# Performance work log

Measured on AMD Instinct MI355X. Metric: run time of the kernel, lower is better.

The kernel has to match this reference:

```python
import jax, jax.numpy as jnp
import numpy as np

HID, NH, QLR, KVLR, QK, VH, RH = 7168, 128, 1536, 512, 128, 128, 64
EPS = 1.1920929e-07  # torch.finfo(float32).eps, RMSNorm eps=None default
ROPE_BASE = 10000.0


def _rmsnorm(x, w):
    return x * jax.lax.rsqrt(jnp.mean(x * x, axis=-1, keepdims=True) + EPS) * w


def _rope_tables(seq_len, dim):
    inv_freq = 1.0 / (ROPE_BASE ** (np.arange(0, dim, 2, dtype=np.float32) / dim))
    t = np.arange(seq_len, dtype=np.float32)
    freqs = np.outer(t, inv_freq)          # [S, dim/2]
    emb = np.concatenate([freqs, freqs], -1)  # [S, dim]
    return jnp.asarray(np.cos(emb)), jnp.asarray(np.sin(emb))


def _apply_rope(x, cos, sin):
    # x: [B, H, S, D]; rotate-half convention matching the torch module
    d = x.shape[-1]
    x1, x2 = x[..., : d // 2], x[..., d // 2 :]
    rotated = jnp.concatenate([-x2, x1], axis=-1)
    return x * cos + rotated * sin


def setup_inputs() -> dict:
    key = jax.random.key(0)
    ks = jax.random.split(key, 9)
    def w(k, out_dim, in_dim):
        return jax.random.normal(k, (out_dim, in_dim), jnp.float32) / np.sqrt(in_dim)
    return {
        "hidden_states": jax.random.normal(ks[0], (1, 1024, HID), jnp.float32),
        "w_q_down": w(ks[1], QLR, HID),
        "q_norm_w": jnp.ones((QLR,), jnp.float32),
        "w_q_up": w(ks[2], NH * (QK + RH), QLR),
        "w_kv_down": w(ks[3], KVLR + RH, HID),
        "kv_norm_w": jnp.ones((KVLR,), jnp.float32),
        "w_kv_up": w(ks[4], NH * (QK + VH), KVLR),
        "w_out": w(ks[5], HID, NH * VH),
    }


def reference(hidden_states, w_q_down, q_norm_w, w_q_up, w_kv_down, kv_norm_w, w_kv_up, w_out):
    B, S, _ = hidden_states.shape
    cos, sin = _rope_tables(S, RH)

    # Q path: down -> RMSNorm -> up, split into non-rope / rope parts
    c_q = jnp.einsum("bsh,qh->bsq", hidden_states, w_q_down)            # [B,S,QLR]
    q_cr = jnp.einsum("bsq,oq->bso", _rmsnorm(c_q, q_norm_w), w_q_up)   # [B,S,NH*(QK+RH)]
    q_cr = q_cr.reshape(B, S, NH, QK + RH).transpose(0, 2, 1, 3)        # [B,NH,S,QK+RH]
    q_c, q_r = q_cr[..., :QK], q_cr[..., QK:]

    # KV path: shared latent + MQA rope key
    ckv_kr = jnp.einsum("bsh,oh->bso", hidden_states, w_kv_down)        # [B,S,KVLR+RH]
    c_kv, k_r = ckv_kr[..., :KVLR], ckv_kr[..., KVLR:]
    k_r = k_r[:, None, :, :]                                            # [B,1,S,RH]
    kv = jnp.einsum("bsq,oq->bso", _rmsnorm(c_kv, kv_norm_w), w_kv_up)  # [B,S,NH*(QK+VH)]
    kv = kv.reshape(B, S, NH, QK + VH).transpose(0, 2, 1, 3)            # [B,NH,S,QK+VH]
    k_c, v = kv[..., :QK], kv[..., QK:]

    q_r = _apply_rope(q_r, cos, sin)
    k_r = _apply_rope(k_r, cos, sin)

    q = jnp.concatenate([q_c, q_r], axis=-1)                            # [B,NH,S,QK+RH]
    k = jnp.concatenate([k_c, jnp.broadcast_to(k_r, (B, NH, S, RH))], axis=-1)

    scale = 1.0 / np.sqrt(QK + RH)
    scores = jnp.einsum("bhqd,bhkd->bhqk", q, k) * scale
    attn = jax.nn.softmax(scores, axis=-1)
    o = jnp.einsum("bhqk,bhkd->bhqd", attn, v)                          # [B,NH,S,VH]
    o = o.transpose(0, 2, 1, 3).reshape(B, S, NH * VH)
    return jnp.einsum("bso,ho->bsh", o, w_out)
```

## Files before the change

kernel.cpp:

```cpp
#include <hip/hip_runtime.h>
#include <hip/hip_bf16.h>
#include <math.h>

#define HIDN 7168
#define NHEAD 128
#define QLRANK 1536
#define KVLRANK 512
#define QKD 128
#define VHD 128
#define RHD 64
#define SEQ 1024
#define RMS_EPS 1.1920929e-07f

typedef unsigned short u16;
typedef __attribute__((ext_vector_type(8))) short bf16x8;
typedef __attribute__((ext_vector_type(4))) float f32x4;
typedef __attribute__((ext_vector_type(8))) unsigned short u16x8;

__device__ __forceinline__ u16 f2bf(float f) {
    unsigned int u = __float_as_uint(f);
    unsigned int r = (u + 0x7FFFu + ((u >> 16) & 1u)) >> 16;
    return (u16)r;
}
__device__ __forceinline__ float bf2f(u16 v) {
    return __uint_as_float(((unsigned int)v) << 16);
}

__device__ __forceinline__ void gld_lds16(const u16* g, u16* l) {
    __builtin_amdgcn_global_load_lds(
        (const __attribute__((address_space(1))) unsigned int*)g,
        (__attribute__((address_space(3))) unsigned int*)l,
        16, 0, 0);
}

__global__ __launch_bounds__(256) void f32_to_bf16(const float* __restrict__ in,
                                                   u16* __restrict__ out, long n) {
    long i = ((long)blockIdx.x * blockDim.x + threadIdx.x) * 8;
    long stride = (long)gridDim.x * blockDim.x * 8;
    for (; i < n; i += stride) {
        float4 a = *(const float4*)(in + i);
        float4 b = *(const float4*)(in + i + 4);
        u16x8 o;
        o[0] = f2bf(a.x); o[1] = f2bf(a.y); o[2] = f2bf(a.z); o[3] = f2bf(a.w);
        o[4] = f2bf(b.x); o[5] = f2bf(b.y); o[6] = f2bf(b.z); o[7] = f2bf(b.w);
        *(u16x8*)(out + i) = o;
    }
}

template <int OUT_BF16>
__global__ __launch_bounds__(256) void gemm_bt(const u16* __restrict__ A,
                                               const u16* __restrict__ B,
                                               void* __restrict__ Cv,
                                               int M, int N, int Kslice, long ldk) {
    __shared__ u16 As[2 * 128 * 64];
    __shared__ u16 Bs[2 * 128 * 64];
    const int tid = threadIdx.x;
    const int lane = tid & 63;
    const int w = tid >> 6;
    const int wr = w >> 1, wc = w & 1;
    const int l15 = lane & 15, lg = lane >> 4;
    const int n0 = blockIdx.x * 128;
    const int m0 = blockIdx.y * 128;
    const long kbase = (long)blockIdx.z * Kslice;

    const u16* asrc[4];
    const u16* bsrc[4];
    int aoff[4];
#pragma unroll
    for (int i = 0; i < 4; ++i) {
        int r = (w * 4 + i) * 8 + (lane >> 3);
        int gc = (lane & 7) ^ (r & 7);
        asrc[i] = A + (long)(m0 + r) * ldk + kbase + gc * 8;
        int br = n0 + r; if (br >= N) br = N - 1;
        bsrc[i] = B + (long)br * ldk + kbase + gc * 8;
        aoff[i] = (w * 4 + i) * 512;
    }

    f32x4 acc[4][4];
    const f32x4 z = {0.f, 0.f, 0.f, 0.f};
#pragma unroll
    for (int i = 0; i < 4; ++i)
#pragma unroll
        for (int j = 0; j < 4; ++j) acc[i][j] = z;

    auto stage = [&](int bufi, int kofs) {
#pragma unroll
        for (int i = 0; i < 4; ++i) {
            gld_lds16(asrc[i] + kofs, As + bufi * 8192 + aoff[i]);
            gld_lds16(bsrc[i] + kofs, Bs + bufi * 8192 + aoff[i]);
        }
    };

    const int nsteps = Kslice >> 6;
    stage(0, 0);
    asm volatile("s_waitcnt vmcnt(0)" ::: "memory");
    __builtin_amdgcn_s_barrier();

    int cur = 0;
    for (int t = 0; t < nsteps; ++t) {
        if (t + 1 < nsteps) stage(cur ^ 1, (t + 1) * 64);
        const u16* Ab = As + cur * 8192;
        const u16* Bb = Bs + cur * 8192;
#pragma unroll
        for (int kk = 0; kk < 2; ++kk) {
            bf16x8 a[4], b[4];
#pragma unroll
            for (int i = 0; i < 4; ++i) {
                int row = wr * 64 + i * 16 + l15;
                a[i] = *(const bf16x8*)&Ab[row * 64 + ((kk * 4 + lg) ^ (row & 7)) * 8];
            }
#pragma unroll
            for (int j = 0; j < 4; ++j) {
                int row = wc * 64 + j * 16 + l15;
                b[j] = *(const bf16x8*)&Bb[row * 64 + ((kk * 4 + lg) ^ (row & 7)) * 8];
            }
#pragma unroll
            for (int i = 0; i < 4; ++i)
#pragma unroll
                for (int j = 0; j < 4; ++j)
                    acc[i][j] = __builtin_amdgcn_mfma_f32_16x16x32_bf16(a[i], b[j], acc[i][j], 0, 0, 0);
        }
        asm volatile("s_waitcnt vmcnt(0)" ::: "memory");
        __builtin_amdgcn_s_barrier();
        cur ^= 1;
    }

#pragma unroll
    for (int i = 0; i < 4; ++i)
#pragma unroll
        for (int j = 0; j < 4; ++j)
#pragma unroll
            for (int r = 0; r < 4; ++r) {
                int m = m0 + wr * 64 + i * 16 + lg * 4 + r;
                int n = n0 + wc * 64 + j * 16 + l15;
                if (n < N) {
                    if (OUT_BF16)
                        ((u16*)Cv)[(long)m * N + n] = f2bf(acc[i][j][r]);
                    else
                        ((float*)Cv)[(long)blockIdx.z * M * N + (long)m * N + n] = acc[i][j][r];
                }
            }
}

__global__ __launch_bounds__(256) void reduce_parts(const float* __restrict__ parts,
                                                    float* __restrict__ out,
                                                    int nparts, long mn) {
    long i = ((long)blockIdx.x * 256 + threadIdx.x) * 4;
    long stride = (long)gridDim.x * 256 * 4;
    for (; i < mn; i += stride) {
        float4 s = *(const float4*)(parts + i);
        for (int p = 1; p < nparts; ++p) {
            float4 v = *(const float4*)(parts + (long)p * mn + i);
            s.x += v.x; s.y += v.y; s.z += v.z; s.w += v.w;
        }
        *(float4*)(out + i) = s;
    }
}

__global__ __launch_bounds__(256) void rmsnorm_kernel(const float* __restrict__ x,
                                                      const float* __restrict__ w,
                                                      u16* __restrict__ y,
                                                      int stride, int norm_len) {
    const int row = blockIdx.x;
    const float* xr = x + (long)row * stride;
    float ss = 0.f;
    for (int i = threadIdx.x; i < norm_len; i += 256) {
        float v = xr[i];
        ss += v * v;
    }
#pragma unroll
    for (int off = 32; off > 0; off >>= 1) ss += __shfl_down(ss, off);
    __shared__ float partial[4];
    if ((threadIdx.x & 63) == 0) partial[threadIdx.x >> 6] = ss;
    __syncthreads();
    float tot = partial[0] + partial[1] + partial[2] + partial[3];
    float rs = 1.0f / sqrtf(tot / (float)norm_len + RMS_EPS);
    u16* yr = y + (long)row * norm_len;
    for (int i = threadIdx.x; i < norm_len; i += 256) yr[i] = f2bf(xr[i] * rs * w[i]);
}

__global__ void rope_tables(float* __restrict__ cos_t, float* __restrict__ sin_t) {
    int s = blockIdx.x;
    int i = threadIdx.x;
    float invf = powf(10000.0f, -((float)(2 * i) / 64.0f));
    float ang = (float)s * invf;
    cos_t[s * 32 + i] = cosf(ang);
    sin_t[s * 32 + i] = sinf(ang);
}

__global__ void rope_q(u16* __restrict__ q_cr, const float* __restrict__ cos_t,
                       const float* __restrict__ sin_t) {
    int s = blockIdx.x;
    int h = blockIdx.y * 2 + (threadIdx.x >> 5);
    int i = threadIdx.x & 31;
    u16* base = q_cr + (s * (NHEAD * 192) + h * 192 + QKD);
    float x1 = bf2f(base[i]);
    float x2 = bf2f(base[i + 32]);
    float c = cos_t[s * 32 + i], sn = sin_t[s * 32 + i];
    base[i]      = f2bf(x1 * c - x2 * sn);
    base[i + 32] = f2bf(x2 * c + x1 * sn);
}

__global__ void rope_k(const float* __restrict__ ckv_kr, const float* __restrict__ cos_t,
                       const float* __restrict__ sin_t, u16* __restrict__ kr) {
    int s = blockIdx.x;
    int i = threadIdx.x;
    if (i < 32) {
        const float* base = ckv_kr + (s * 576 + 512);
        float x1 = base[i], x2 = base[i + 32];
        float c = cos_t[s * 32 + i], sn = sin_t[s * 32 + i];
        kr[s * 64 + i]      = f2bf(x1 * c - x2 * sn);
        kr[s * 64 + i + 32] = f2bf(x2 * c + x1 * sn);
    }
}

__global__ __launch_bounds__(256) void build_vt(const u16* __restrict__ kv,
                                                u16* __restrict__ vT) {
    __shared__ u16 vtile[64][136];
    const int h = blockIdx.x, sb = blockIdx.y, s0 = sb * 64;
    const int tid = threadIdx.x;
#pragma unroll
    for (int it = 0; it < 4; ++it) {
        int c = it * 256 + tid;
        int row = c >> 4;
        int off8 = (c & 15) * 8;
        *(u16x8*)&vtile[row][off8] =
            *(const u16x8*)&kv[(s0 + row) * 32768 + h * 256 + 128 + off8];
    }
    __syncthreads();
    const int sl = tid & 63;
    const int dvb = tid >> 6;
#pragma unroll
    for (int it = 0; it < 32; ++it) {
        int dv = dvb + it * 4;
        vT[(h * 128 + dv) * 1024 + s0 + sl] = vtile[sl][dv];
    }
}

__global__ __launch_bounds__(512) void mla_attn(const u16* __restrict__ q_cr,
                                                const u16* __restrict__ kv,
                                                const u16* __restrict__ kr,
                                                const u16* __restrict__ vT,
                                                u16* __restrict__ o_g) {
    __shared__ u16 ks[64][200];
    __shared__ u16 vts[128][72];
    __shared__ u16 p_lds[8][16][72];
    const int qb = blockIdx.x, h = blockIdx.y;
    const int s0q = qb * 128;
    const int tid = threadIdx.x, lane = tid & 63, w = tid >> 6;
    const int l15 = lane & 15, lg = lane >> 4;
    const float scale = 0.07216878364870323f;

    bf16x8 qreg[6];
    {
        const int qrow = s0q + w * 16 + l15;
#pragma unroll
        for (int kk = 0; kk < 6; ++kk)
            qreg[kk] = *(const bf16x8*)&q_cr[qrow * (NHEAD * 192) + h * 192 + kk * 32 + lg * 8];
    }

    const int krow0 = tid >> 4,           koff0 = (tid & 15) * 8;
    const int krow1 = (512 + tid) >> 4,   koff1 = ((512 + tid) & 15) * 8;
    const int rrow  = tid >> 3,           roff  = (tid & 7) * 8;
    const int vdv0  = tid >> 3,           voff0 = (tid & 7) * 8;
    const int vdv1  = (512 + tid) >> 3,   voff1 = ((512 + tid) & 7) * 8;
    const u16* kvp = kv + h * 256;
    const u16* vtp = vT + (long)(h * 128) * 1024;

    u16x8 kreg0, kreg1, krreg, vreg0, vreg1;
    auto load_tile = [&](int s0k) {
        kreg0 = *(const u16x8*)&kvp[(long)(s0k + krow0) * 32768 + koff0];
        kreg1 = *(const u16x8*)&kvp[(long)(s0k + krow1) * 32768 + koff1];
        krreg = *(const u16x8*)&kr[(s0k + rrow) * 64 + roff];
        vreg0 = *(const u16x8*)&vtp[(long)vdv0 * 1024 + s0k + voff0];
        vreg1 = *(const u16x8*)&vtp[(long)vdv1 * 1024 + s0k + voff1];
    };

    f32x4 o_acc[8];
    const f32x4 z = {0.f, 0.f, 0.f, 0.f};
#pragma unroll
    for (int d = 0; d < 8; ++d) o_acc[d] = z;
    float m_r[4], l_r[4];
#pragma unroll
    for (int r = 0; r < 4; ++r) { m_r[r] = -1e30f; l_r[r] = 0.f; }

    load_tile(0);

    for (int kt = 0; kt < 16; ++kt) {
        __syncthreads();
        *(u16x8*)&ks[krow0][koff0]      = kreg0;
        *(u16x8*)&ks[krow1][koff1]      = kreg1;
        *(u16x8*)&ks[rrow][128 + roff]  = krreg;
        *(u16x8*)&vts[vdv0][voff0]      = vreg0;
        *(u16x8*)&vts[vdv1][voff1]      = vreg1;
        __syncthreads();
        if (kt + 1 < 16) load_tile((kt + 1) * 64);

        f32x4 sf[4];
#pragma unroll
        for (int j = 0; j < 4; ++j) sf[j] = z;
#pragma unroll
        for (int kk = 0; kk < 6; ++kk) {
            bf16x8 a = qreg[kk];
#pragma unroll
            for (int j = 0; j < 4; ++j) {
                bf16x8 b = *(const bf16x8*)&ks[j * 16 + l15][kk * 32 + lg * 8];
                sf[j] = __builtin_amdgcn_mfma_f32_16x16x32_bf16(a, b, sf[j], 0, 0, 0);
            }
        }

        float p[4][4];
        float alpha[4];
#pragma unroll
        for (int r = 0; r < 4; ++r) {
            float mx = fmaxf(fmaxf(sf[0][r], sf[1][r]), fmaxf(sf[2][r], sf[3][r]));
#pragma unroll
            for (int off = 1; off < 16; off <<= 1) mx = fmaxf(mx, __shfl_xor(mx, off));
            mx *= scale;
            float mnew = fmaxf(m_r[r], mx);
            alpha[r] = __expf(m_r[r] - mnew);
            float rs = 0.f;
#pragma unroll
            for (int j = 0; j < 4; ++j) {
                float pv = __expf(sf[j][r] * scale - mnew);
                p[j][r] = pv;
                rs += pv;
            }
#pragma unroll
            for (int off = 1; off < 16; off <<= 1) rs += __shfl_xor(rs, off);
            l_r[r] = l_r[r] * alpha[r] + rs;
            m_r[r] = mnew;
        }
#pragma unroll
        for (int d = 0; d < 8; ++d)
#pragma unroll
            for (int r = 0; r < 4; ++r) o_acc[d][r] *= alpha[r];

#pragma unroll
        for (int j = 0; j < 4; ++j)
#pragma unroll
            for (int r = 0; r < 4; ++r)
                p_lds[w][lg * 4 + r][j * 16 + l15] = f2bf(p[j][r]);

#pragma unroll
        for (int kk2 = 0; kk2 < 2; ++kk2) {
            bf16x8 a = *(const bf16x8*)&p_lds[w][l15][kk2 * 32 + lg * 8];
#pragma unroll
            for (int d = 0; d < 8; ++d) {
                bf16x8 b = *(const bf16x8*)&vts[d * 16 + l15][kk2 * 32 + lg * 8];
                o_acc[d] = __builtin_amdgcn_mfma_f32_16x16x32_bf16(a, b, o_acc[d], 0, 0, 0);
            }
        }
    }

#pragma unroll
    for (int d = 0; d < 8; ++d)
#pragma unroll
        for (int r = 0; r < 4; ++r) {
            int srow = s0q + w * 16 + lg * 4 + r;
            float v = o_acc[d][r] / l_r[r];
            o_g[srow * 16384 + h * 128 + d * 16 + l15] = f2bf(v);
        }
}

extern "C" void kernel_launch(void* const* d_in, const int* in_sizes, int n_in,
                              void* d_out, int out_size, void* d_ws, size_t ws_size,
                              hipStream_t stream) {
    const float* hs        = (const float*)d_in[0];
    const float* w_q_down  = (const float*)d_in[1];
    const float* q_norm_w  = (const float*)d_in[2];
    const float* w_q_up    = (const float*)d_in[3];
    const float* w_kv_down = (const float*)d_in[4];
    const float* kv_norm_w = (const float*)d_in[5];
    const float* w_kv_up   = (const float*)d_in[6];
    const float* w_out     = (const float*)d_in[7];
    float* out = (float*)d_out;
    char* ws = (char*)d_ws;

    const size_t SZ_HS   = (size_t)SEQ * HIDN * 2;
    const size_t SZ_KV   = (size_t)SEQ * 32768 * 2;
    const size_t SZ_QCR  = (size_t)SEQ * (NHEAD * 192) * 2;
    const size_t SZ_VT   = (size_t)NHEAD * 128 * 1024 * 2;
    const size_t SZ_WB   = (size_t)24576 * 1536 * 2;
    const size_t SZ_CQ   = (size_t)SEQ * QLRANK * 4;
    const size_t SZ_CQN  = (size_t)SEQ * QLRANK * 2;
    const size_t SZ_CKV  = (size_t)SEQ * 576 * 4;
    const size_t SZ_CKVN = (size_t)SEQ * KVLRANK * 2;
    const size_t SZ_KR   = (size_t)SEQ * 64 * 2;
    const size_t SZ_OG   = (size_t)SEQ * 16384 * 2;
    const size_t SZ_TAB  = (size_t)SEQ * 32 * 4;

    size_t off = 0;
    u16* hs_bf  = (u16*)(ws + off); off += SZ_HS;
    u16* kvb    = (u16*)(ws + off); off += SZ_KV;
    u16* q_cr   = (u16*)(ws + off); off += SZ_QCR;
    u16* vT     = (u16*)(ws + off); off += SZ_VT;
    u16* W_BUF  = (u16*)(ws + off); off += SZ_WB;
    float* parts = (float*)((char*)W_BUF + 33554432);
    u16* wout_bf = (u16*)ws;
    float* c_q    = (float*)(ws + off); off += SZ_CQ;
    u16* cq_n     = (u16*)(ws + off); off += SZ_CQN;
    float* ckv_kr = (float*)(ws + off); off += SZ_CKV;
    u16* ckv_n    = (u16*)(ws + off); off += SZ_CKVN;
    u16* kr       = (u16*)(ws + off); off += SZ_KR;
    u16* o_g      = (u16*)(ws + off); off += SZ_OG;
    float* cos_t  = (float*)(ws + off); off += SZ_TAB;
    float* sin_t  = (float*)(ws + off); off += SZ_TAB;
    const size_t SZ_POP = (size_t)2 * SEQ * HIDN * 4;
    float* parts_op = (float*)(ws + off);
    const bool splitOP = (off + SZ_POP) <= ws_size;
    (void)in_sizes; (void)n_in; (void)out_size;

    rope_tables<<<dim3(SEQ), dim3(32), 0, stream>>>(cos_t, sin_t);
    f32_to_bf16<<<2048, 256, 0, stream>>>(hs, hs_bf, (long)SEQ * HIDN);

    f32_to_bf16<<<2048, 256, 0, stream>>>(w_q_down, W_BUF, (long)QLRANK * HIDN);
    gemm_bt<0><<<dim3(QLRANK / 128, SEQ / 128, 4), 256, 0, stream>>>(hs_bf, W_BUF, parts, SEQ, QLRANK, HIDN / 4, HIDN);
    reduce_parts<<<1024, 256, 0, stream>>>(parts, c_q, 4, (long)SEQ * QLRANK);
    rmsnorm_kernel<<<SEQ, 256, 0, stream>>>(c_q, q_norm_w, cq_n, QLRANK, QLRANK);

    f32_to_bf16<<<2048, 256, 0, stream>>>(w_q_up, W_BUF, (long)24576 * QLRANK);
    gemm_bt<1><<<dim3(24576 / 128, SEQ / 128), 256, 0, stream>>>(cq_n, W_BUF, q_cr, SEQ, 24576, QLRANK, QLRANK);

    f32_to_bf16<<<2048, 256, 0, stream>>>(w_kv_down, W_BUF, (long)576 * HIDN);
    gemm_bt<0><<<dim3(5, SEQ / 128, 8), 256, 0, stream>>>(hs_bf, W_BUF, parts, SEQ, 576, HIDN / 8, HIDN);
    reduce_parts<<<1024, 256, 0, stream>>>(parts, ckv_kr, 8, (long)SEQ * 576);
    rmsnorm_kernel<<<SEQ, 256, 0, stream>>>(ckv_kr, kv_norm_w, ckv_n, 576, KVLRANK);
    rope_k<<<SEQ, 64, 0, stream>>>(ckv_kr, cos_t, sin_t, kr);

    f32_to_bf16<<<2048, 256, 0, stream>>>(w_kv_up, W_BUF, (long)32768 * KVLRANK);
    gemm_bt<1><<<dim3(32768 / 128, SEQ / 128), 256, 0, stream>>>(ckv_n, W_BUF, kvb, SEQ, 32768, KVLRANK, KVLRANK);

    rope_q<<<dim3(SEQ, NHEAD / 2), 64, 0, stream>>>(q_cr, cos_t, sin_t);
    build_vt<<<dim3(NHEAD, SEQ / 64), 256, 0, stream>>>(kvb, vT);

    mla_attn<<<dim3(SEQ / 128, NHEAD), 512, 0, stream>>>(q_cr, kvb, kr, vT, o_g);

    f32_to_bf16<<<2048, 256, 0, stream>>>(w_out, wout_bf, (long)HIDN * 16384);
    if (splitOP) {
        gemm_bt<0><<<dim3(HIDN / 128, SEQ / 128, 2), 256, 0, stream>>>(o_g, wout_bf, parts_op, SEQ, HIDN, 16384 / 2, 16384);
        reduce_parts<<<1024, 256, 0, stream>>>(parts_op, out, 2, (long)SEQ * HIDN);
    } else {
        gemm_bt<0><<<dim3(HIDN / 128, SEQ / 128), 256, 0, stream>>>(o_g, wout_bf, out, SEQ, HIDN, 16384, 16384);
    }
}
```

Baseline: 1.022 ms.

## Deepen GEMM LDS pipeline to four stages and drop split-K for out-proj

The shared GEMM kernel moves from a double-buffered LDS pipeline to a four-buffer ring. Three k-tiles stay in flight, and partial vmcnt waits replace the full drain on every iteration, so more global-load latency is hidden. The output projection no longer uses the 2-way split-K with a separate reduction pass and writes straight to the output. The weight conversion grid for that projection is also enlarged. LDS use per block grows to 128KB, which may limit occupancy to one block per CU.

```diff
diff --git a/kernel.cpp b/kernel.cpp
--- a/kernel.cpp
+++ b/kernel.cpp
@@ -52,8 +52,8 @@
                                                const u16* __restrict__ B,
                                                void* __restrict__ Cv,
                                                int M, int N, int Kslice, long ldk) {
-    __shared__ u16 As[2 * 128 * 64];
-    __shared__ u16 Bs[2 * 128 * 64];
+    __shared__ u16 As[4 * 128 * 64];
+    __shared__ u16 Bs[4 * 128 * 64];
     const int tid = threadIdx.x;
     const int lane = tid & 63;
     const int w = tid >> 6;
@@ -83,24 +83,30 @@
 #pragma unroll
         for (int j = 0; j < 4; ++j) acc[i][j] = z;
 
-    auto stage = [&](int bufi, int kofs) {
+    auto stage = [&](int t) {
+        const int bb = (t & 3) * 8192;
+        const long ko = (long)t * 64;
 #pragma unroll
         for (int i = 0; i < 4; ++i) {
-            gld_lds16(asrc[i] + kofs, As + bufi * 8192 + aoff[i]);
-            gld_lds16(bsrc[i] + kofs, Bs + bufi * 8192 + aoff[i]);
+            gld_lds16(asrc[i] + ko, As + bb + aoff[i]);
+            gld_lds16(bsrc[i] + ko, Bs + bb + aoff[i]);
         }
     };
 
     const int nsteps = Kslice >> 6;
-    stage(0, 0);
-    asm volatile("s_waitcnt vmcnt(0)" ::: "memory");
-    __builtin_amdgcn_s_barrier();
-
-    int cur = 0;
+    stage(0);
+    if (1 < nsteps) stage(1);
+    if (2 < nsteps) stage(2);
+
     for (int t = 0; t < nsteps; ++t) {
-        if (t + 1 < nsteps) stage(cur ^ 1, (t + 1) * 64);
-        const u16* Ab = As + cur * 8192;
-        const u16* Bb = Bs + cur * 8192;
+        if (t + 2 < nsteps)      asm volatile("s_waitcnt vmcnt(16)" ::: "memory");
+        else if (t + 1 < nsteps) asm volatile("s_waitcnt vmcnt(8)" ::: "memory");
+        else                     asm volatile("s_waitcnt vmcnt(0)" ::: "memory");
+        __builtin_amdgcn_s_barrier();
+        __builtin_amdgcn_sched_barrier(0);
+        if (t + 3 < nsteps) stage(t + 3);
+        const u16* Ab = As + (t & 3) * 8192;
+        const u16* Bb = Bs + (t & 3) * 8192;
 #pragma unroll
         for (int kk = 0; kk < 2; ++kk) {
             bf16x8 a[4], b[4];
@@ -120,9 +126,6 @@
                 for (int j = 0; j < 4; ++j)
                     acc[i][j] = __builtin_amdgcn_mfma_f32_16x16x32_bf16(a[i], b[j], acc[i][j], 0, 0, 0);
         }
-        asm volatile("s_waitcnt vmcnt(0)" ::: "memory");
-        __builtin_amdgcn_s_barrier();
-        cur ^= 1;
     }
 
 #pragma unroll
@@ -406,10 +409,7 @@
     u16* o_g      = (u16*)(ws + off); off += SZ_OG;
     float* cos_t  = (float*)(ws + off); off += SZ_TAB;
     float* sin_t  = (float*)(ws + off); off += SZ_TAB;
-    const size_t SZ_POP = (size_t)2 * SEQ * HIDN * 4;
-    float* parts_op = (float*)(ws + off);
-    const bool splitOP = (off + SZ_POP) <= ws_size;
-    (void)in_sizes; (void)n_in; (void)out_size;
+    (void)in_sizes; (void)n_in; (void)out_size; (void)ws_size;
 
     rope_tables<<<dim3(SEQ), dim3(32), 0, stream>>>(cos_t, sin_t);
     f32_to_bf16<<<2048, 256, 0, stream>>>(hs, hs_bf, (long)SEQ * HIDN);
@@ -436,11 +436,6 @@
 
     mla_attn<<<dim3(SEQ / 128, NHEAD), 512, 0, stream>>>(q_cr, kvb, kr, vT, o_g);
 
-    f32_to_bf16<<<2048, 256, 0, stream>>>(w_out, wout_bf, (long)HIDN * 16384);
-    if (splitOP) {
-        gemm_bt<0><<<dim3(HIDN / 128, SEQ / 128, 2), 256, 0, stream>>>(o_g, wout_bf, parts_op, SEQ, HIDN, 16384 / 2, 16384);
-        reduce_parts<<<1024, 256, 0, stream>>>(parts_op, out, 2, (long)SEQ * HIDN);
-    } else {
-        gemm_bt<0><<<dim3(HIDN / 128, SEQ / 128), 256, 0, stream>>>(o_g, wout_bf, out, SEQ, HIDN, 16384, 16384);
-    }
-}
+    f32_to_bf16<<<4096, 256, 0, stream>>>(w_out, wout_bf, (long)HIDN * 16384);
+    gemm_bt<0><<<dim3(HIDN / 128, SEQ / 128), 256, 0, stream>>>(o_g, wout_bf, out, SEQ, HIDN, 16384, 16384);
+}
```

Result: slower. 1.443 ms (+41.1%).
